# Performance work log

Measured on AMD Instinct MI355X. Metric: run time of the kernel, lower is better.

## Reference

```python
import jax, jax.numpy as jnp
import numpy as np

T, B, D, H = 2048, 2, 1024, 16
DPH = D // H
SCALE = DPH ** -0.5


def setup_inputs() -> dict:
    key = jax.random.key(0)
    ks = jax.random.split(key, 5)
    x = jax.random.normal(ks[0], (T, B, D), dtype=jnp.float32)
    Wk = jax.random.normal(ks[1], (D, D), dtype=jnp.float32) * 0.02
    Wv = jax.random.normal(ks[2], (D, D), dtype=jnp.float32) * 0.02
    Wq = jax.random.normal(ks[3], (D, D), dtype=jnp.float32) * 0.02
    Wo = jax.random.normal(ks[4], (D, D), dtype=jnp.float32) * 0.02
    # causal mask: True marks positions to hide (masked_fill semantics)
    mask = jnp.triu(jnp.ones((T, T), dtype=bool), k=1)
    return {"x": x, "Wk": Wk, "Wv": Wv, "Wq": Wq, "Wo": Wo, "mask": mask}


def _split_heads(y):
    # 't b (d h) -> b h t d' : d_per_head is the OUTER factor of the split
    t, b, _ = y.shape
    return y.reshape(t, b, DPH, H).transpose(1, 3, 0, 2)  # [b, h, t, d]


def reference(x, Wk, Wv, Wq, Wo, mask):
    # nn.Linear(bias=False): y = x @ W.T
    k = _split_heads(x @ Wk.T)
    v = _split_heads(x @ Wv.T)
    q = _split_heads(x @ Wq.T)
    scores = jnp.einsum('bhid,bhjd->bhij', q, k) * SCALE  # [b,h,t,t]
    scores = jnp.where(mask, -jnp.inf, scores)
    attn = jax.nn.softmax(scores, axis=-1)
    # dropout is identity in eval mode
    out = jnp.einsum('bhij,bhjd->bhid', attn, v)  # [b,h,t,d]
    # 'b h t d -> t b (h d)' : heads are the OUTER factor of the merge
    out = out.transpose(2, 0, 1, 3).reshape(x.shape[0], x.shape[1], D)
    return out @ Wo.T
```

## Files before the change

kernel.cpp:

```cpp
#include <hip/hip_runtime.h>

#define T_LEN   2048
#define BATCH   2
#define DMODEL  1024
#define NHEAD   16
#define DHEAD   64
#define MROWS   4096
#define KDIM    1024
#define NDIM    1024
#define ATT_SC2 (0.125f * 1.44269504088896f)

typedef unsigned short u16;
typedef unsigned int   u32;
typedef u16   u16x8 __attribute__((ext_vector_type(8)));
typedef u16   u16x4 __attribute__((ext_vector_type(4)));
typedef __bf16 bf16x8 __attribute__((ext_vector_type(8)));
typedef float f32x4 __attribute__((ext_vector_type(4)));

__device__ __forceinline__ u16 f2bf(float f) {
  u32 u = __builtin_bit_cast(u32, f);
  u += 0x7fffu + ((u >> 16) & 1u);
  return (u16)(u >> 16);
}

__device__ __forceinline__ u16 bfc(float f) {
  return __builtin_bit_cast(u16, (__bf16)f);
}

__device__ __forceinline__ f32x4 mfma16(u16x8 a, u16x8 b, f32x4 c) {
  return __builtin_amdgcn_mfma_f32_16x16x32_bf16(
      __builtin_bit_cast(bf16x8, a), __builtin_bit_cast(bf16x8, b), c, 0, 0, 0);
}

__device__ __forceinline__ void gload16(const u16* g, u16* l) {
  __builtin_amdgcn_global_load_lds((const __attribute__((address_space(1))) void*)g,
                                   (__attribute__((address_space(3))) void*)l,
                                   16, 0, 0);
}

#define XN 4194304u
__global__ __launch_bounds__(256) void cast_all(
    const float* __restrict__ x,  const float* __restrict__ wk,
    const float* __restrict__ wv, const float* __restrict__ wq,
    const float* __restrict__ wo, u16* __restrict__ ws) {
  size_t i = ((size_t)blockIdx.x * 256 + threadIdx.x) * 4;
  const float* src; size_t soff, doff; float sc = 1.0f;
  if (i < XN) {
    int m = (int)(i >> 10), d = (int)(i & 1023);
    int t = m >> 1, b = m & 1;
    src = x; soff = i;
    doff = ((size_t)(b * 2048 + t) << 10) + d;
  } else {
    size_t off = i - XN;
    int wi = (int)(off >> 20);
    off &= 1048575u;
    int u = (int)(off >> 10), c = (int)(off & 1023);
    src = (wi == 0) ? wk : (wi == 1) ? wv : (wi == 2) ? wq : wo;
    soff = off;
    if (wi == 3) {
      doff = XN + 3u * 1048576u + off;
    } else {
      int slot = (wi == 2) ? 0 : (wi == 0) ? 1 : 2;
      int up = (u & 15) * 64 + (u >> 4);
      doff = XN + (size_t)slot * 1048576u + ((size_t)up << 10) + c;
      if (wi == 2) sc = ATT_SC2;
    }
  }
  float4 v = *reinterpret_cast<const float4*>(src + soff);
  u16x4 o;
  o.s0 = f2bf(v.x * sc); o.s1 = f2bf(v.y * sc); o.s2 = f2bf(v.z * sc); o.s3 = f2bf(v.w * sc);
  *reinterpret_cast<u16x4*>(ws + doff) = o;
}

__global__ __launch_bounds__(256, 2) void gemm_qkv(
    const u16* __restrict__ xbm, const u16* __restrict__ Wqkv,
    u16* __restrict__ Qh, u16* __restrict__ Kh, u16* __restrict__ Vt) {
  __shared__ __align__(16) u16 As[256 * 64];
  __shared__ __align__(16) u16 Bs[128 * 64];

  const int tid = threadIdx.x;
  const int l  = tid & 63, w = tid >> 6;
  const int lr = l & 15,  lg = l >> 4;
  const int wm = w >> 1,  wn = w & 1;

  const int blk  = blockIdx.x;
  const int wgid = (blk & 7) * 48 + (blk >> 3);

  const u16 *A, *W;
  int m0, n0, isV;
  if (wgid < 256) {
    const int bx = wgid >> 4, by = wgid & 15;
    A = xbm; W = Wqkv; m0 = by * 256; n0 = bx * 128; isV = 0;
  } else {
    const int v = wgid - 256;
    const int vby = v >> 5, vbx = v & 31;
    A = Wqkv + (2048u << 10); W = xbm; m0 = vby * 256; n0 = vbx * 128; isV = 1;
  }

  f32x4 acc[8][4];
#pragma unroll
  for (int i = 0; i < 8; ++i)
#pragma unroll
    for (int j = 0; j < 4; ++j) acc[i][j] = (f32x4)(0.0f);

  for (int k0 = 0; k0 < KDIM; k0 += 64) {
#pragma unroll
    for (int i = 0; i < 8; ++i) {
      const int base = i * 256 + w * 64;
      const int p = base + l;
      const int r = p >> 3, c = p & 7;
      gload16(A + (size_t)(m0 + r) * KDIM + k0 + ((c ^ (r & 7)) << 3),
              As + (size_t)base * 8);
    }
#pragma unroll
    for (int i = 0; i < 4; ++i) {
      const int base = i * 256 + w * 64;
      const int p = base + l;
      const int r = p >> 3, c = p & 7;
      gload16(W + (size_t)(n0 + r) * KDIM + k0 + ((c ^ (r & 7)) << 3),
              Bs + (size_t)base * 8);
    }
    __syncthreads();

#pragma unroll
    for (int ks = 0; ks < 2; ++ks) {
      const int cr = ks * 4 + lg;
      u16x8 bf_[4];
#pragma unroll
      for (int ni = 0; ni < 4; ++ni) {
        const int rr = wn * 64 + ni * 16 + lr;
        bf_[ni] = *reinterpret_cast<const u16x8*>(Bs + rr * 64 + ((cr ^ (rr & 7)) << 3));
      }
      __builtin_amdgcn_s_setprio(1);
#pragma unroll
      for (int mi = 0; mi < 8; ++mi) {
        const int rr = wm * 128 + mi * 16 + lr;
        const u16x8 af = *reinterpret_cast<const u16x8*>(
            As + rr * 64 + ((cr ^ (rr & 7)) << 3));
#pragma unroll
        for (int ni = 0; ni < 4; ++ni)
          acc[mi][ni] = mfma16(af, bf_[ni], acc[mi][ni]);
      }
      __builtin_amdgcn_s_setprio(0);
    }
    __syncthreads();
  }

#pragma unroll
  for (int mi = 0; mi < 8; ++mi)
#pragma unroll
    for (int ni = 0; ni < 4; ++ni)
#pragma unroll
      for (int r = 0; r < 4; ++r) {
        const int row = m0 + wm * 128 + mi * 16 + lg * 4 + r;
        const int col = n0 + wn * 64 + ni * 16 + lr;
        const u16 v = bfc(acc[mi][ni][r]);
        if (!isV) {
          const int bb = row >> 11, t = row & 2047;
          const int c = col & 1023, hh = c >> 6, dp = c & 63;
          u16* d = (col < 1024) ? Qh : Kh;
          d[(((size_t)(bb * NHEAD + hh) << 11) + t) * 64 + dp] = v;
        } else {
          const int hh = row >> 6, dp = row & 63;
          const int bb = col >> 11, t = col & 2047;
          Vt[((((size_t)(bb * NHEAD + hh)) * 64 + dp) << 11) + t] = v;
        }
      }
}

__global__ __launch_bounds__(256) void gemm_o(
    const u16* __restrict__ A, const u16* __restrict__ W, float* __restrict__ out) {
  __shared__ __align__(16) u16 As[128 * 64];
  __shared__ __align__(16) u16 Bs[64 * 64];

  const int tid = threadIdx.x;
  const int l  = tid & 63, w = tid >> 6;
  const int lr = l & 15,  lg = l >> 4;
  const int wm = w >> 1,  wn = w & 1;

  const int blk  = blockIdx.x;
  const int wgid = (blk & 7) * 64 + (blk >> 3);
  const int bx = wgid >> 5, by = wgid & 31;
  const int m0 = by * 128;
  const int n0 = bx * 64;

  f32x4 acc[4][2];
#pragma unroll
  for (int i = 0; i < 4; ++i)
#pragma unroll
    for (int j = 0; j < 2; ++j) acc[i][j] = (f32x4)(0.0f);

  for (int k0 = 0; k0 < KDIM; k0 += 64) {
#pragma unroll
    for (int i = 0; i < 4; ++i) {
      const int base = i * 256 + w * 64;
      const int p = base + l;
      const int r = p >> 3, c = p & 7;
      gload16(A + (size_t)(m0 + r) * KDIM + k0 + ((c ^ (r & 7)) << 3),
              As + (size_t)base * 8);
    }
#pragma unroll
    for (int i = 0; i < 2; ++i) {
      const int base = i * 256 + w * 64;
      const int p = base + l;
      const int r = p >> 3, c = p & 7;
      gload16(W + (size_t)(n0 + r) * KDIM + k0 + ((c ^ (r & 7)) << 3),
              Bs + (size_t)base * 8);
    }
    __syncthreads();

#pragma unroll
    for (int ks = 0; ks < 2; ++ks) {
      const int cr = ks * 4 + lg;
      u16x8 bf_[2];
#pragma unroll
      for (int ni = 0; ni < 2; ++ni) {
        const int rr = wn * 32 + ni * 16 + lr;
        bf_[ni] = *reinterpret_cast<const u16x8*>(Bs + rr * 64 + ((cr ^ (rr & 7)) << 3));
      }
      __builtin_amdgcn_s_setprio(1);
#pragma unroll
      for (int mi = 0; mi < 4; ++mi) {
        const int rr = wm * 64 + mi * 16 + lr;
        const u16x8 af = *reinterpret_cast<const u16x8*>(
            As + rr * 64 + ((cr ^ (rr & 7)) << 3));
#pragma unroll
        for (int ni = 0; ni < 2; ++ni)
          acc[mi][ni] = mfma16(af, bf_[ni], acc[mi][ni]);
      }
      __builtin_amdgcn_s_setprio(0);
    }
    __syncthreads();
  }

#pragma unroll
  for (int mi = 0; mi < 4; ++mi)
#pragma unroll
    for (int ni = 0; ni < 2; ++ni)
#pragma unroll
      for (int r = 0; r < 4; ++r) {
        const int row = m0 + wm * 64 + mi * 16 + lg * 4 + r;
        const int col = n0 + wn * 32 + ni * 16 + lr;
        const int t = row & 2047, bb = row >> 11;
        out[((size_t)(t * 2 + bb) << 10) + col] = acc[mi][ni][r];
      }
}

__global__ __launch_bounds__(256, 2) void attn_fwd(
    const u16* __restrict__ Qh, const u16* __restrict__ Kh,
    const u16* __restrict__ Vt, u16* __restrict__ Aout) {
  __shared__ __align__(16) u16 smem[36864];

  const int tid = threadIdx.x;
  const int l = tid & 63, w = tid >> 6;
  const int lr = l & 15, lg = l >> 4;
  const int wk = w & 1, wq = w >> 1;
  const int blk = blockIdx.x;
  const int bxx = (blk >> 3) & 15;
  const int bh  = ((blk >> 7) << 3) + (blk & 7);
  const int b = bh >> 4, h = bh & 15;

  const u16* kg = Kh + ((size_t)bh << 17);
  const u16* vg = Vt + ((size_t)bh << 17);
  u16* Pw = smem + 32768 + w * 1024;

  float* redO = reinterpret_cast<float*>(smem);
  float* redS = reinterpret_cast<float*>(smem + 32768);

  const u16x8 ones = {0x3F80,0x3F80,0x3F80,0x3F80,0x3F80,0x3F80,0x3F80,0x3F80};

  auto stage = [&](int buf, int kv0) {
    u16* kb = smem + buf * 8192;
    u16* vb = smem + 16384 + buf * 8192;
#pragma unroll
    for (int j = 0; j < 4; ++j) {
      const int base = (j * 4 + w) * 64;
      const int gg = base + l;
      const int rk = gg >> 3, ck = gg & 7;
      gload16(kg + (size_t)(kv0 + rk) * 64 + ((ck ^ (rk & 7)) << 3),
              kb + (size_t)base * 8);
      const int rv = gg >> 4, cv = gg & 15;
      gload16(vg + ((size_t)rv << 11) + kv0 + ((cv ^ (rv & 15)) << 3),
              vb + (size_t)base * 8);
    }
  };

  for (int ph = 0; ph < 2; ++ph) {
    const int qb = ph ? bxx : 31 - bxx;
    const int qbw = qb * 64 + wq * 32;

    u16x8 qf[2][2];
#pragma unroll
    for (int g = 0; g < 2; ++g) {
      const int qrow = qbw + g * 16 + lr;
      const u16* qptr = Qh + (((size_t)bh << 11) + qrow) * 64 + lg * 8;
      qf[g][0] = *reinterpret_cast<const u16x8*>(qptr);
      qf[g][1] = *reinterpret_cast<const u16x8*>(qptr + 32);
    }

    f32x4 oacc[2][4];
#pragma unroll
    for (int g = 0; g < 2; ++g)
#pragma unroll
      for (int i = 0; i < 4; ++i) oacc[g][i] = (f32x4)(0.0f);
    f32x4 sum4[2] = {(f32x4)(0.0f), (f32x4)(0.0f)};

    const int npair = (qb + 2) >> 1;
    stage(0, 0);
    __syncthreads();

    int cur = 0;
    for (int t = 0; t < npair; ++t) {
      const int kv0 = t * 128;
      const bool pf = (t + 1 < npair);
      if (pf) {
        stage(cur ^ 1, kv0 + 128);
        asm volatile("s_waitcnt vmcnt(8)" ::: "memory");
      } else {
        asm volatile("s_waitcnt vmcnt(0)" ::: "memory");
      }
      __builtin_amdgcn_sched_barrier(0);
      __builtin_amdgcn_s_barrier();

      const int kvw = kv0 + wk * 64;
      if (kvw <= qbw + 31) {
        const u16* kb = smem + cur * 8192;
        const u16* vb = smem + 16384 + cur * 8192;

        u16x8 kf[4][2];
#pragma unroll
        for (int tt = 0; tt < 4; ++tt) {
          const int row = wk * 64 + tt * 16 + lr;
          kf[tt][0] = *reinterpret_cast<const u16x8*>(
              kb + row * 64 + ((lg ^ (row & 7)) << 3));
          kf[tt][1] = *reinterpret_cast<const u16x8*>(
              kb + row * 64 + (((4 + lg) ^ (row & 7)) << 3));
        }
        u16x8 vf[2][4];
#pragma unroll
        for (int kh = 0; kh < 2; ++kh)
#pragma unroll
          for (int ni = 0; ni < 4; ++ni) {
            const int dr = ni * 16 + lr;
            const int ck = wk * 8 + kh * 4 + lg;
            vf[kh][ni] = *reinterpret_cast<const u16x8*>(
                vb + dr * 128 + ((ck ^ (dr & 15)) << 3));
          }

#pragma unroll
        for (int g = 0; g < 2; ++g) {
          const int qbg = qbw + g * 16;
          if (kvw <= qbg + 15) {
            const bool diag = (kvw + 63 > qbg);
            const int qrow = qbg + lr;

            __builtin_amdgcn_s_setprio(1);
#pragma unroll
            for (int tt = 0; tt < 4; ++tt) {
              f32x4 sacc = (f32x4)(0.0f);
              sacc = mfma16(kf[tt][0], qf[g][0], sacc);
              sacc = mfma16(kf[tt][1], qf[g][1], sacc);
              u16x4 pk;
#pragma unroll
              for (int r = 0; r < 4; ++r) {
                const int kv = kvw + tt * 16 + lg * 4 + r;
                const float s = (diag && kv > qrow) ? -1e30f : sacc[r];
                pk[r] = bfc(__builtin_amdgcn_exp2f(s - 8.0f));
              }
              *reinterpret_cast<u16x4*>(
                  &Pw[lr * 64 + (((tt * 2 + (lg >> 1)) ^ (lr & 7)) << 3)
                      + ((lg & 1) << 2)]) = pk;
            }

#pragma unroll
            for (int kh = 0; kh < 2; ++kh) {
              const u16x8 pa = *reinterpret_cast<const u16x8*>(
                  &Pw[lr * 64 + (((kh * 4 + lg) ^ (lr & 7)) << 3)]);
              sum4[g] = mfma16(pa, ones, sum4[g]);
#pragma unroll
              for (int ni = 0; ni < 4; ++ni)
                oacc[g][ni] = mfma16(pa, vf[kh][ni], oacc[g][ni]);
            }
            __builtin_amdgcn_s_setprio(0);
          }
        }
      }

      asm volatile("s_waitcnt lgkmcnt(0)" ::: "memory");
      __builtin_amdgcn_sched_barrier(0);
      __builtin_amdgcn_s_barrier();
      cur ^= 1;
    }

    if (wk) {
      float* po = redO + wq * 2176;
#pragma unroll
      for (int g = 0; g < 2; ++g) {
#pragma unroll
        for (int ni = 0; ni < 4; ++ni)
#pragma unroll
          for (int r = 0; r < 4; ++r)
            po[(g * 16 + lg * 4 + r) * 68 + ni * 16 + lr] = oacc[g][ni][r];
        if (lr == 0) {
#pragma unroll
          for (int r = 0; r < 4; ++r)
            redS[wq * 32 + g * 16 + lg * 4 + r] = sum4[g][r];
        }
      }
    }
    __syncthreads();

    if (!wk) {
      const float* po = redO + wq * 2176;
#pragma unroll
      for (int g = 0; g < 2; ++g) {
        f32x4 ss = sum4[g];
#pragma unroll
        for (int r = 0; r < 4; ++r)
          ss[r] += redS[wq * 32 + g * 16 + lg * 4 + r];
#pragma unroll
        for (int r = 0; r < 4; ++r) {
          const float inv = 1.0f / ss[r];
          const int q = qbw + g * 16 + lg * 4 + r;
          const size_t rowbase = (((size_t)(b * 2048 + q)) << 10) + h * DHEAD;
#pragma unroll
          for (int ni = 0; ni < 4; ++ni)
            Aout[rowbase + ni * 16 + lr] = bfc(
                (oacc[g][ni][r] + po[(g * 16 + lg * 4 + r) * 68 + ni * 16 + lr])
                * inv);
        }
      }
    }
    __syncthreads();
  }
}

extern "C" void kernel_launch(void* const* d_in, const int* in_sizes, int n_in,
                              void* d_out, int out_size, void* d_ws, size_t ws_size,
                              hipStream_t stream) {
  const float* x  = (const float*)d_in[0];
  const float* Wk = (const float*)d_in[1];
  const float* Wv = (const float*)d_in[2];
  const float* Wq = (const float*)d_in[3];
  const float* Wo = (const float*)d_in[4];

  u16* ws   = (u16*)d_ws;
  u16* xbm  = ws;
  u16* Wqkv = xbm + 4194304;
  u16* Wob  = Wqkv + 3145728;
  u16* Qh   = Wob + 1048576;
  u16* Kh   = Qh  + 4194304;
  u16* Vt   = Kh  + 4194304;
  u16* Aout = Vt  + 4194304;

  cast_all<<<8192, 256, 0, stream>>>(x, Wk, Wv, Wq, Wo, ws);

  gemm_qkv<<<384, 256, 0, stream>>>(xbm, Wqkv, Qh, Kh, Vt);

  attn_fwd<<<512, 256, 0, stream>>>(Qh, Kh, Vt, Aout);

  gemm_o<<<512, 256, 0, stream>>>(Aout, Wob, (float*)d_out);
}
```

Baseline: 107.3 us.

## Switch attention to 32x32 MFMA with in-register P via permlane swap

Rewrites the attention inner loop to use 32x32x16 bf16 MFMA for both QK^T and PV instead of 16x16x32 tiles. Score probabilities are packed to bf16 in registers with v_cvt_pk_bf16_f32 and rearranged with v_permlane32_swap, so the per-wave LDS round trip for P is no longer needed. The row sum is taken with VALU adds plus a shuffle instead of an extra MFMA against a ones vector. This aims to cut LDS traffic, MFMA issue count and LDS footprint. In exchange it raises register pressure from the 16-wide accumulators and reads V fragments from LDS inside the inner loop.

```diff
diff --git a/kernel.cpp b/kernel.cpp
--- a/kernel.cpp
+++ b/kernel.cpp
@@ -14,8 +14,10 @@
 typedef unsigned int   u32;
 typedef u16   u16x8 __attribute__((ext_vector_type(8)));
 typedef u16   u16x4 __attribute__((ext_vector_type(4)));
+typedef u32   u32x4 __attribute__((ext_vector_type(4)));
 typedef __bf16 bf16x8 __attribute__((ext_vector_type(8)));
-typedef float f32x4 __attribute__((ext_vector_type(4)));
+typedef float f32x4  __attribute__((ext_vector_type(4)));
+typedef float f32x16 __attribute__((ext_vector_type(16)));
 
 __device__ __forceinline__ u16 f2bf(float f) {
   u32 u = __builtin_bit_cast(u32, f);
@@ -30,6 +32,26 @@
 __device__ __forceinline__ f32x4 mfma16(u16x8 a, u16x8 b, f32x4 c) {
   return __builtin_amdgcn_mfma_f32_16x16x32_bf16(
       __builtin_bit_cast(bf16x8, a), __builtin_bit_cast(bf16x8, b), c, 0, 0, 0);
+}
+
+__device__ __forceinline__ f32x16 mfma32(u16x8 a, u16x8 b, f32x16 c) {
+  return __builtin_amdgcn_mfma_f32_32x32x16_bf16(
+      __builtin_bit_cast(bf16x8, a), __builtin_bit_cast(bf16x8, b), c, 0, 0, 0);
+}
+
+__device__ __forceinline__ f32x16 mfma32p(u32x4 a, u16x8 b, f32x16 c) {
+  return __builtin_amdgcn_mfma_f32_32x32x16_bf16(
+      __builtin_bit_cast(bf16x8, a), __builtin_bit_cast(bf16x8, b), c, 0, 0, 0);
+}
+
+__device__ __forceinline__ u32 cvtpk(float lo, float hi) {
+  u32 r;
+  asm("v_cvt_pk_bf16_f32 %0, %1, %2" : "=v"(r) : "v"(lo), "v"(hi));
+  return r;
+}
+
+__device__ __forceinline__ void pswap(u32& a, u32& b) {
+  asm volatile("v_permlane32_swap_b32 %0, %1" : "+v"(a), "+v"(b));
 }
 
 __device__ __forceinline__ void gload16(const u16* g, u16* l) {
@@ -249,11 +271,11 @@
 __global__ __launch_bounds__(256, 2) void attn_fwd(
     const u16* __restrict__ Qh, const u16* __restrict__ Kh,
     const u16* __restrict__ Vt, u16* __restrict__ Aout) {
-  __shared__ __align__(16) u16 smem[36864];
+  __shared__ __align__(16) u16 smem[32768];
 
   const int tid = threadIdx.x;
   const int l = tid & 63, w = tid >> 6;
-  const int lr = l & 15, lg = l >> 4;
+  const int l31 = l & 31, hi = l >> 5;
   const int wk = w & 1, wq = w >> 1;
   const int blk = blockIdx.x;
   const int bxx = (blk >> 3) & 15;
@@ -262,12 +284,9 @@
 
   const u16* kg = Kh + ((size_t)bh << 17);
   const u16* vg = Vt + ((size_t)bh << 17);
-  u16* Pw = smem + 32768 + w * 1024;
 
   float* redO = reinterpret_cast<float*>(smem);
-  float* redS = reinterpret_cast<float*>(smem + 32768);
-
-  const u16x8 ones = {0x3F80,0x3F80,0x3F80,0x3F80,0x3F80,0x3F80,0x3F80,0x3F80};
+  float* redS = redO + 4352;
 
   auto stage = [&](int buf, int kv0) {
     u16* kb = smem + buf * 8192;
@@ -288,22 +307,16 @@
   for (int ph = 0; ph < 2; ++ph) {
     const int qb = ph ? bxx : 31 - bxx;
     const int qbw = qb * 64 + wq * 32;
-
-    u16x8 qf[2][2];
-#pragma unroll
-    for (int g = 0; g < 2; ++g) {
-      const int qrow = qbw + g * 16 + lr;
-      const u16* qptr = Qh + (((size_t)bh << 11) + qrow) * 64 + lg * 8;
-      qf[g][0] = *reinterpret_cast<const u16x8*>(qptr);
-      qf[g][1] = *reinterpret_cast<const u16x8*>(qptr + 32);
-    }
-
-    f32x4 oacc[2][4];
-#pragma unroll
-    for (int g = 0; g < 2; ++g)
-#pragma unroll
-      for (int i = 0; i < 4; ++i) oacc[g][i] = (f32x4)(0.0f);
-    f32x4 sum4[2] = {(f32x4)(0.0f), (f32x4)(0.0f)};
+    const int q31 = qbw + l31;
+
+    const u16* qptr = Qh + (((size_t)bh << 11) + q31) * 64 + hi * 8;
+    u16x8 qf[4];
+#pragma unroll
+    for (int ks = 0; ks < 4; ++ks)
+      qf[ks] = *reinterpret_cast<const u16x8*>(qptr + ks * 16);
+
+    f32x16 acc0 = (f32x16)(0.0f), acc1 = (f32x16)(0.0f);
+    float sumw = 0.0f;
 
     const int npair = (qb + 2) >> 1;
     stage(0, 0);
@@ -327,61 +340,62 @@
         const u16* kb = smem + cur * 8192;
         const u16* vb = smem + 16384 + cur * 8192;
 
-        u16x8 kf[4][2];
-#pragma unroll
-        for (int tt = 0; tt < 4; ++tt) {
-          const int row = wk * 64 + tt * 16 + lr;
-          kf[tt][0] = *reinterpret_cast<const u16x8*>(
-              kb + row * 64 + ((lg ^ (row & 7)) << 3));
-          kf[tt][1] = *reinterpret_cast<const u16x8*>(
-              kb + row * 64 + (((4 + lg) ^ (row & 7)) << 3));
-        }
-        u16x8 vf[2][4];
-#pragma unroll
-        for (int kh = 0; kh < 2; ++kh)
-#pragma unroll
-          for (int ni = 0; ni < 4; ++ni) {
-            const int dr = ni * 16 + lr;
-            const int ck = wk * 8 + kh * 4 + lg;
-            vf[kh][ni] = *reinterpret_cast<const u16x8*>(
-                vb + dr * 128 + ((ck ^ (dr & 15)) << 3));
-          }
-
-#pragma unroll
-        for (int g = 0; g < 2; ++g) {
-          const int qbg = qbw + g * 16;
-          if (kvw <= qbg + 15) {
-            const bool diag = (kvw + 63 > qbg);
-            const int qrow = qbg + lr;
-
+#pragma unroll
+        for (int tile = 0; tile < 2; ++tile) {
+          const int tb = kvw + tile * 32;
+          if (tb <= qbw + 31) {
+            f32x16 s16 = (f32x16)(0.0f);
             __builtin_amdgcn_s_setprio(1);
 #pragma unroll
-            for (int tt = 0; tt < 4; ++tt) {
-              f32x4 sacc = (f32x4)(0.0f);
-              sacc = mfma16(kf[tt][0], qf[g][0], sacc);
-              sacc = mfma16(kf[tt][1], qf[g][1], sacc);
-              u16x4 pk;
-#pragma unroll
-              for (int r = 0; r < 4; ++r) {
-                const int kv = kvw + tt * 16 + lg * 4 + r;
-                const float s = (diag && kv > qrow) ? -1e30f : sacc[r];
-                pk[r] = bfc(__builtin_amdgcn_exp2f(s - 8.0f));
-              }
-              *reinterpret_cast<u16x4*>(
-                  &Pw[lr * 64 + (((tt * 2 + (lg >> 1)) ^ (lr & 7)) << 3)
-                      + ((lg & 1) << 2)]) = pk;
-            }
-
-#pragma unroll
-            for (int kh = 0; kh < 2; ++kh) {
-              const u16x8 pa = *reinterpret_cast<const u16x8*>(
-                  &Pw[lr * 64 + (((kh * 4 + lg) ^ (lr & 7)) << 3)]);
-              sum4[g] = mfma16(pa, ones, sum4[g]);
-#pragma unroll
-              for (int ni = 0; ni < 4; ++ni)
-                oacc[g][ni] = mfma16(pa, vf[kh][ni], oacc[g][ni]);
+            for (int ks = 0; ks < 4; ++ks) {
+              const int row = wk * 64 + tile * 32 + l31;
+              const u16x8 kf = *reinterpret_cast<const u16x8*>(
+                  kb + row * 64 + (((2 * ks + hi) ^ (row & 7)) << 3));
+              s16 = mfma32(kf, qf[ks], s16);
             }
             __builtin_amdgcn_s_setprio(0);
+
+            const bool diag = (tb + 31 > qbw);
+#pragma unroll
+            for (int i = 0; i < 16; ++i) {
+              float s = s16[i];
+              if (diag) {
+                const int kv = tb + (i & 3) + 8 * (i >> 2) + 4 * hi;
+                if (kv > q31) s = -1e30f;
+              }
+              s16[i] = __builtin_amdgcn_exp2f(s - 8.0f);
+            }
+            float ts = 0.0f;
+#pragma unroll
+            for (int i = 0; i < 16; ++i) ts += s16[i];
+            sumw += ts;
+
+#pragma unroll
+            for (int ks2 = 0; ks2 < 2; ++ks2) {
+              const int pb = ks2 * 8;
+              u32 a0 = cvtpk(s16[pb + 0], s16[pb + 1]);
+              u32 b0 = cvtpk(s16[pb + 4], s16[pb + 5]);
+              u32 a1 = cvtpk(s16[pb + 2], s16[pb + 3]);
+              u32 b1 = cvtpk(s16[pb + 6], s16[pb + 7]);
+              pswap(a0, b0);
+              pswap(a1, b1);
+              u32x4 pa;
+              pa.x = a0; pa.y = a1; pa.z = b0; pa.w = b1;
+
+              const int cc = wk * 8 + tile * 4 + ks2 * 2 + hi;
+              __builtin_amdgcn_s_setprio(1);
+              {
+                const int dr0 = l31;
+                const u16x8 vf0 = *reinterpret_cast<const u16x8*>(
+                    vb + dr0 * 128 + ((cc ^ (dr0 & 15)) << 3));
+                acc0 = mfma32p(pa, vf0, acc0);
+                const int dr1 = 32 + l31;
+                const u16x8 vf1 = *reinterpret_cast<const u16x8*>(
+                    vb + dr1 * 128 + ((cc ^ (dr1 & 15)) << 3));
+                acc1 = mfma32p(pa, vf1, acc1);
+              }
+              __builtin_amdgcn_s_setprio(0);
+            }
           }
         }
       }
@@ -392,43 +406,32 @@
       cur ^= 1;
     }
 
+    const float sfull = sumw + __shfl_xor(sumw, 32, 64);
+
     if (wk) {
       float* po = redO + wq * 2176;
 #pragma unroll
-      for (int g = 0; g < 2; ++g) {
-#pragma unroll
-        for (int ni = 0; ni < 4; ++ni)
-#pragma unroll
-          for (int r = 0; r < 4; ++r)
-            po[(g * 16 + lg * 4 + r) * 68 + ni * 16 + lr] = oacc[g][ni][r];
-        if (lr == 0) {
-#pragma unroll
-          for (int r = 0; r < 4; ++r)
-            redS[wq * 32 + g * 16 + lg * 4 + r] = sum4[g][r];
-        }
-      }
+      for (int i = 0; i < 16; ++i) {
+        const int qr = (i & 3) + 8 * (i >> 2) + 4 * hi;
+        po[qr * 68 + l31]      = acc0[i];
+        po[qr * 68 + 32 + l31] = acc1[i];
+      }
+      if (l < 32) redS[wq * 32 + l] = sfull;
     }
     __syncthreads();
 
     if (!wk) {
       const float* po = redO + wq * 2176;
-#pragma unroll
-      for (int g = 0; g < 2; ++g) {
-        f32x4 ss = sum4[g];
-#pragma unroll
-        for (int r = 0; r < 4; ++r)
-          ss[r] += redS[wq * 32 + g * 16 + lg * 4 + r];
-#pragma unroll
-        for (int r = 0; r < 4; ++r) {
-          const float inv = 1.0f / ss[r];
-          const int q = qbw + g * 16 + lg * 4 + r;
-          const size_t rowbase = (((size_t)(b * 2048 + q)) << 10) + h * DHEAD;
-#pragma unroll
-          for (int ni = 0; ni < 4; ++ni)
-            Aout[rowbase + ni * 16 + lr] = bfc(
-                (oacc[g][ni][r] + po[(g * 16 + lg * 4 + r) * 68 + ni * 16 + lr])
-                * inv);
-        }
+      const float ssT  = sfull + redS[wq * 32 + l31];
+      const float invL = 1.0f / ssT;
+#pragma unroll
+      for (int i = 0; i < 16; ++i) {
+        const int qr = (i & 3) + 8 * (i >> 2) + 4 * hi;
+        const float inv = __shfl(invL, qr, 64);
+        const int q = qbw + qr;
+        const size_t rb = (((size_t)(b * 2048 + q)) << 10) + h * DHEAD;
+        Aout[rb + l31]      = bfc((acc0[i] + po[qr * 68 + l31]) * inv);
+        Aout[rb + 32 + l31] = bfc((acc1[i] + po[qr * 68 + 32 + l31]) * inv);
       }
     }
     __syncthreads();
```

New measurement: 107.9 us. About the same (+0.5%).

## Split attention KV tile across four waves per query group with 512-thread blocks

Applied to the files above, without the earlier changes.

The attention kernel doubles its block from 4 to 8 waves. Each block tile now splits its 128 KV columns across four waves of 32 keys each, instead of two waves of 64. Per-wave K/V fragments, the P scratch buffer (now unswizzled, stride 40) and the staging loop shrink to match. Partial outputs and row sums from three waves are reduced through shared memory, which adds reduction traffic and tighter register limits in exchange for more waves to hide latency.

```diff
diff --git a/kernel.cpp b/kernel.cpp
--- a/kernel.cpp
+++ b/kernel.cpp
@@ -246,15 +246,15 @@
       }
 }
 
-__global__ __launch_bounds__(256, 2) void attn_fwd(
+__global__ __launch_bounds__(512, 2) void attn_fwd(
     const u16* __restrict__ Qh, const u16* __restrict__ Kh,
     const u16* __restrict__ Vt, u16* __restrict__ Aout) {
-  __shared__ __align__(16) u16 smem[36864];
+  __shared__ __align__(16) u16 smem[37888];
 
   const int tid = threadIdx.x;
   const int l = tid & 63, w = tid >> 6;
   const int lr = l & 15, lg = l >> 4;
-  const int wk = w & 1, wq = w >> 1;
+  const int wk = w & 3, wq = w >> 2;
   const int blk = blockIdx.x;
   const int bxx = (blk >> 3) & 15;
   const int bh  = ((blk >> 7) << 3) + (blk & 7);
@@ -262,7 +262,7 @@
 
   const u16* kg = Kh + ((size_t)bh << 17);
   const u16* vg = Vt + ((size_t)bh << 17);
-  u16* Pw = smem + 32768 + w * 1024;
+  u16* Pw = smem + 32768 + w * 640;
 
   float* redO = reinterpret_cast<float*>(smem);
   float* redS = reinterpret_cast<float*>(smem + 32768);
@@ -273,8 +273,8 @@
     u16* kb = smem + buf * 8192;
     u16* vb = smem + 16384 + buf * 8192;
 #pragma unroll
-    for (int j = 0; j < 4; ++j) {
-      const int base = (j * 4 + w) * 64;
+    for (int j = 0; j < 2; ++j) {
+      const int base = (j * 8 + w) * 64;
       const int gg = base + l;
       const int rk = gg >> 3, ck = gg & 7;
       gload16(kg + (size_t)(kv0 + rk) * 64 + ((ck ^ (rk & 7)) << 3),
@@ -315,48 +315,46 @@
       const bool pf = (t + 1 < npair);
       if (pf) {
         stage(cur ^ 1, kv0 + 128);
-        asm volatile("s_waitcnt vmcnt(8)" ::: "memory");
+        asm volatile("s_waitcnt vmcnt(4)" ::: "memory");
       } else {
         asm volatile("s_waitcnt vmcnt(0)" ::: "memory");
       }
       __builtin_amdgcn_sched_barrier(0);
       __builtin_amdgcn_s_barrier();
 
-      const int kvw = kv0 + wk * 64;
+      const int kvw = kv0 + wk * 32;
       if (kvw <= qbw + 31) {
         const u16* kb = smem + cur * 8192;
         const u16* vb = smem + 16384 + cur * 8192;
 
-        u16x8 kf[4][2];
-#pragma unroll
-        for (int tt = 0; tt < 4; ++tt) {
-          const int row = wk * 64 + tt * 16 + lr;
+        u16x8 kf[2][2];
+#pragma unroll
+        for (int tt = 0; tt < 2; ++tt) {
+          const int row = wk * 32 + tt * 16 + lr;
           kf[tt][0] = *reinterpret_cast<const u16x8*>(
               kb + row * 64 + ((lg ^ (row & 7)) << 3));
           kf[tt][1] = *reinterpret_cast<const u16x8*>(
               kb + row * 64 + (((4 + lg) ^ (row & 7)) << 3));
         }
-        u16x8 vf[2][4];
-#pragma unroll
-        for (int kh = 0; kh < 2; ++kh)
-#pragma unroll
-          for (int ni = 0; ni < 4; ++ni) {
-            const int dr = ni * 16 + lr;
-            const int ck = wk * 8 + kh * 4 + lg;
-            vf[kh][ni] = *reinterpret_cast<const u16x8*>(
-                vb + dr * 128 + ((ck ^ (dr & 15)) << 3));
-          }
+        u16x8 vf[4];
+#pragma unroll
+        for (int ni = 0; ni < 4; ++ni) {
+          const int dr = ni * 16 + lr;
+          const int ck = wk * 4 + lg;
+          vf[ni] = *reinterpret_cast<const u16x8*>(
+              vb + dr * 128 + ((ck ^ (dr & 15)) << 3));
+        }
 
 #pragma unroll
         for (int g = 0; g < 2; ++g) {
           const int qbg = qbw + g * 16;
           if (kvw <= qbg + 15) {
-            const bool diag = (kvw + 63 > qbg);
+            const bool diag = (kvw + 31 > qbg);
             const int qrow = qbg + lr;
 
             __builtin_amdgcn_s_setprio(1);
 #pragma unroll
-            for (int tt = 0; tt < 4; ++tt) {
+            for (int tt = 0; tt < 2; ++tt) {
               f32x4 sacc = (f32x4)(0.0f);
               sacc = mfma16(kf[tt][0], qf[g][0], sacc);
               sacc = mfma16(kf[tt][1], qf[g][1], sacc);
@@ -367,19 +365,15 @@
                 const float s = (diag && kv > qrow) ? -1e30f : sacc[r];
                 pk[r] = bfc(__builtin_amdgcn_exp2f(s - 8.0f));
               }
-              *reinterpret_cast<u16x4*>(
-                  &Pw[lr * 64 + (((tt * 2 + (lg >> 1)) ^ (lr & 7)) << 3)
-                      + ((lg & 1) << 2)]) = pk;
+              *reinterpret_cast<u16x4*>(&Pw[lr * 40 + tt * 16 + lg * 4]) = pk;
             }
 
-#pragma unroll
-            for (int kh = 0; kh < 2; ++kh) {
-              const u16x8 pa = *reinterpret_cast<const u16x8*>(
-                  &Pw[lr * 64 + (((kh * 4 + lg) ^ (lr & 7)) << 3)]);
+            {
+              const u16x8 pa = *reinterpret_cast<const u16x8*>(&Pw[lr * 40 + lg * 8]);
               sum4[g] = mfma16(pa, ones, sum4[g]);
 #pragma unroll
               for (int ni = 0; ni < 4; ++ni)
-                oacc[g][ni] = mfma16(pa, vf[kh][ni], oacc[g][ni]);
+                oacc[g][ni] = mfma16(pa, vf[ni], oacc[g][ni]);
             }
             __builtin_amdgcn_s_setprio(0);
           }
@@ -393,7 +387,7 @@
     }
 
     if (wk) {
-      float* po = redO + wq * 2176;
+      float* po = redO + (wq * 3 + wk - 1) * 2176;
 #pragma unroll
       for (int g = 0; g < 2; ++g) {
 #pragma unroll
@@ -404,30 +398,34 @@
         if (lr == 0) {
 #pragma unroll
           for (int r = 0; r < 4; ++r)
-            redS[wq * 32 + g * 16 + lg * 4 + r] = sum4[g][r];
+            redS[(wq * 3 + wk - 1) * 32 + g * 16 + lg * 4 + r] = sum4[g][r];
         }
       }
     }
     __syncthreads();
 
     if (!wk) {
-      const float* po = redO + wq * 2176;
 #pragma unroll
       for (int g = 0; g < 2; ++g) {
         f32x4 ss = sum4[g];
 #pragma unroll
-        for (int r = 0; r < 4; ++r)
-          ss[r] += redS[wq * 32 + g * 16 + lg * 4 + r];
+        for (int j = 0; j < 3; ++j)
+#pragma unroll
+          for (int r = 0; r < 4; ++r)
+            ss[r] += redS[(wq * 3 + j) * 32 + g * 16 + lg * 4 + r];
 #pragma unroll
         for (int r = 0; r < 4; ++r) {
           const float inv = 1.0f / ss[r];
           const int q = qbw + g * 16 + lg * 4 + r;
           const size_t rowbase = (((size_t)(b * 2048 + q)) << 10) + h * DHEAD;
 #pragma unroll
-          for (int ni = 0; ni < 4; ++ni)
-            Aout[rowbase + ni * 16 + lr] = bfc(
-                (oacc[g][ni][r] + po[(g * 16 + lg * 4 + r) * 68 + ni * 16 + lr])
-                * inv);
+          for (int ni = 0; ni < 4; ++ni) {
+            float o = oacc[g][ni][r];
+#pragma unroll
+            for (int j = 0; j < 3; ++j)
+              o += redO[(wq * 3 + j) * 2176 + (g * 16 + lg * 4 + r) * 68 + ni * 16 + lr];
+            Aout[rowbase + ni * 16 + lr] = bfc(o * inv);
+          }
         }
       }
     }
@@ -457,7 +455,7 @@
 
   gemm_qkv<<<384, 256, 0, stream>>>(xbm, Wqkv, Qh, Kh, Vt);
 
-  attn_fwd<<<512, 256, 0, stream>>>(Qh, Kh, Vt, Aout);
+  attn_fwd<<<512, 512, 0, stream>>>(Qh, Kh, Vt, Aout);
 
   gemm_o<<<512, 256, 0, stream>>>(Aout, Wob, (float*)d_out);
 }
```

New measurement: 118.9 us. +10.8%, slower.
